# Optimization experiments

Measured on AMD Instinct MI355X. Metric: run time of the kernel, lower is better.

The kernel has to match this reference:

```python
import jax, jax.numpy as jnp
import numpy as np

LAYERS = 30
LPS = 10            # layers per stack (layers // stacks)
K = 3               # kernel size
RC = 64             # residual channels
GC = 128            # gate channels
SC = 64             # skip channels
AC = 80             # aux (mel) channels
DN = ('NCH', 'OIH', 'NCH')


def _conv1x1(w, x):
    # w: (O, I), x: (B, I, T) -> (B, O, T)
    return jnp.einsum('oi,bit->bot', w, x)


def setup_inputs() -> dict:
    key = jax.random.key(0)
    ks = jax.random.split(key, 10)
    B, T = 8, 8192
    s = 0.05
    f32 = jnp.float32
    inp = {
        'x': jax.random.normal(ks[0], (B, 1, T), f32),
        'x_mask': jnp.ones((B, 1, T), f32),
        'c': jax.random.normal(ks[1], (B, AC, T), f32),
        'first_w': jax.random.normal(ks[2], (RC, 1, 1), f32) * s,
        'first_b': jnp.zeros((RC,), f32),
        'conv_w': jax.random.normal(ks[3], (LAYERS, GC, RC, K), f32) * s,
        'conv_b': jnp.zeros((LAYERS, GC), f32),
        'aux_w': jax.random.normal(ks[4], (LAYERS, GC, AC), f32) * s,
        'out_w': jax.random.normal(ks[5], (LAYERS, RC + SC, GC // 2), f32) * s,
        'out_b': jnp.zeros((LAYERS, RC + SC), f32),
        'last_w1': jax.random.normal(ks[6], (SC, SC), f32) * s,
        'last_b1': jnp.zeros((SC,), f32),
        'last_w2': jax.random.normal(ks[7], (1, SC), f32) * s,
        'last_b2': jnp.zeros((1,), f32),
    }
    return inp


def reference(x, x_mask, c, first_w, first_b, conv_w, conv_b, aux_w,
              out_w, out_b, last_w1, last_b1, last_w2, last_b2):
    # first 1x1 conv: (B,1,T) -> (B,RC,T)
    x = jax.lax.conv_general_dilated(x, first_w, (1,), [(0, 0)],
                                     dimension_numbers=DN) + first_b[None, :, None]
    skips = jnp.zeros_like(x[:, :SC])  # (B, SC, T)
    for l in range(LAYERS):
        d = 2 ** (l % LPS)
        pad = (K - 1) // 2 * d
        residual = x
        # dilated conv (same padding): (B,RC,T) -> (B,GC,T)
        h = jax.lax.conv_general_dilated(x, conv_w[l], (1,), [(pad, pad)],
                                         rhs_dilation=(d,), dimension_numbers=DN)
        h = h + conv_b[l][None, :, None]
        # local conditioning 1x1 (no bias)
        h = h + _conv1x1(aux_w[l], c)
        xa, xb = jnp.split(h, 2, axis=1)          # (B, GC/2, T) each
        z = jnp.tanh(xa) * jax.nn.sigmoid(xb)     # gated activation
        o = _conv1x1(out_w[l], z) + out_b[l][None, :, None]  # (B, RC+SC, T)
        o = o * x_mask
        x = residual + o[:, :RC]
        skips = skips + o[:, RC:]
    # last_conv: ReLU -> 1x1 -> ReLU -> 1x1
    y = jax.nn.relu(skips)
    y = _conv1x1(last_w1, y) + last_b1[None, :, None]
    y = jax.nn.relu(y)
    y = _conv1x1(last_w2, y) + last_b2[None, :, None]
    return y
```

## Files before the change

### kernel.cpp

```cpp
#include <hip/hip_runtime.h>
#include <hip/hip_bf16.h>
#include <stdint.h>

#define T_LEN 8192
#define LAYERS 30

typedef __attribute__((ext_vector_type(8))) short bfx8;
typedef __attribute__((ext_vector_type(4))) float fx4;
typedef __attribute__((ext_vector_type(4))) int ix4;

static __device__ __forceinline__ unsigned short f2bf(float f) {
    union { float fv; unsigned u; } v; v.fv = f;
    unsigned r = v.u + 0x7fffu + ((v.u >> 16) & 1u);
    return (unsigned short)(r >> 16);
}
static __device__ __forceinline__ float bf2f(unsigned short u) {
    union { unsigned u; float f; } v; v.u = ((unsigned)u) << 16;
    return v.f;
}
static __device__ __forceinline__ unsigned pack2(float a, float b) {
    return (unsigned)f2bf(a) | ((unsigned)f2bf(b) << 16);
}

__global__ void pack_weights_k(const float* __restrict__ conv_w,
                               const float* __restrict__ aux_w,
                               const float* __restrict__ out_w,
                               unsigned short* __restrict__ wpack) {
    int tid = blockIdx.x * 256 + threadIdx.x;
    int lane = tid & 63;
    int f = (tid >> 6) % 88;
    int l = tid / (88 * 64);
    unsigned short vals[8];
#pragma unroll
    for (int j = 0; j < 8; j++) {
        int kl = ((lane >> 4) * 8) + j;
        float v;
        if (f < 72) {
            int ks = f >> 3, nf = f & 7;
            int g = nf * 16 + (lane & 15);
            if (ks < 6) {
                int tap = ks >> 1;
                int i = (ks & 1) * 32 + kl;
                v = conv_w[((l * 128 + g) * 64 + i) * 3 + tap];
            } else {
                int a = (ks - 6) * 32 + kl;
                v = (a < 80) ? aux_w[(l * 128 + g) * 80 + a] : 0.f;
            }
        } else {
            int fo = f - 72;
            int ks = fo >> 3, nf = fo & 7;
            int p = nf * 16 + (lane & 15);
            v = out_w[(l * 128 + p) * 64 + ks * 32 + kl];
        }
        vals[j] = f2bf(v);
    }
    unsigned* dst = (unsigned*)(wpack + (size_t)tid * 8);
    dst[0] = (unsigned)vals[0] | ((unsigned)vals[1] << 16);
    dst[1] = (unsigned)vals[2] | ((unsigned)vals[3] << 16);
    dst[2] = (unsigned)vals[4] | ((unsigned)vals[5] << 16);
    dst[3] = (unsigned)vals[6] | ((unsigned)vals[7] << 16);
}

__global__ void prep_c_k(const float* __restrict__ c, unsigned short* __restrict__ cbf) {
    __shared__ float tile[80][65];
    int bid = blockIdx.x;
    int b = bid >> 7;
    int t0 = (bid & 127) << 6;
    for (int idx = threadIdx.x; idx < 80 * 64; idx += 256) {
        int a = idx >> 6, tt = idx & 63;
        tile[a][tt] = c[((size_t)(b * 80 + a)) * T_LEN + t0 + tt];
    }
    __syncthreads();
    for (int idx = threadIdx.x; idx < 64 * 96; idx += 256) {
        int tt = idx / 96, a = idx % 96;
        float v = (a < 80) ? tile[a][tt] : 0.f;
        cbf[((size_t)(b * T_LEN + t0 + tt)) * 96 + a] = f2bf(v);
    }
}

__global__ __launch_bounds__(256, 4) void layer_k(
    const float* __restrict__ xsrc,
    float* __restrict__ xdst,
    unsigned short* __restrict__ skipbf,
    const unsigned short* __restrict__ cbf,
    const float* __restrict__ xmask,
    const float* __restrict__ fw, const float* __restrict__ fb,
    const unsigned short* __restrict__ wl,
    const float* __restrict__ conv_b_l,
    const float* __restrict__ out_b_l,
    int d, int first)
{
    __shared__ char smem[40960];
    unsigned short* xtap  = (unsigned short*)smem;
    float*          sg_l  = (float*)smem;
    unsigned short* z_l   = (unsigned short*)(smem + 17408);
    float*          o_l   = (float*)smem;
    unsigned short* ctile = (unsigned short*)(smem + 27648);

    const int tid = threadIdx.x;
    const int lane = tid & 63;
    const int wv = tid >> 6;
    int bid = (((int)blockIdx.x & 7) * 128) + ((int)blockIdx.x >> 3);
    const int b = bid >> 7;
    const int t0 = (bid & 127) << 6;
    const long rowbase = (long)b * T_LEN;
    const int klane = (lane >> 4) * 8;
    const int mrow = lane & 15;
    const int trow = (lane >> 4) * 4;
    const int tq_t = tid >> 2;
    const int tq_q = tid & 3;

    float xc[16];
    if (first) {
        float xs = xsrc[rowbase + t0 + tq_t];
#pragma unroll
        for (int k = 0; k < 16; k++)
            xc[k] = fmaf(fw[tq_q * 16 + k], xs, fb[tq_q * 16 + k]);
    } else {
        const float4* src = (const float4*)(xsrc + ((rowbase + t0 + tq_t) << 6) + tq_q * 16);
#pragma unroll
        for (int k = 0; k < 4; k++) {
            float4 v = src[k];
            xc[k * 4] = v.x; xc[k * 4 + 1] = v.y; xc[k * 4 + 2] = v.z; xc[k * 4 + 3] = v.w;
        }
    }
    {
        unsigned pk[8];
#pragma unroll
        for (int k = 0; k < 8; k++) pk[k] = pack2(xc[k * 2], xc[k * 2 + 1]);
        unsigned short* dst = xtap + (64 + tq_t) * 72 + tq_q * 16;
        *(ix4*)dst       = *(const ix4*)&pk[0];
        *(ix4*)(dst + 8) = *(const ix4*)&pk[4];
    }
#pragma unroll
    for (int u = 0; u < 2; u++) {
        int idx = tid + u * 256;
        int tp = idx >> 8;
        int rem = idx & 255;
        int row = rem >> 2, qq = rem & 3;
        int tg = t0 + row + (tp ? d : -d);
        float hv[16];
        if ((unsigned)tg < (unsigned)T_LEN) {
            if (first) {
                float xs = xsrc[rowbase + tg];
#pragma unroll
                for (int k = 0; k < 16; k++)
                    hv[k] = fmaf(fw[qq * 16 + k], xs, fb[qq * 16 + k]);
            } else {
                const float4* src = (const float4*)(xsrc + ((rowbase + tg) << 6) + qq * 16);
#pragma unroll
                for (int k = 0; k < 4; k++) {
                    float4 v = src[k];
                    hv[k * 4] = v.x; hv[k * 4 + 1] = v.y; hv[k * 4 + 2] = v.z; hv[k * 4 + 3] = v.w;
                }
            }
        } else {
#pragma unroll
            for (int k = 0; k < 16; k++) hv[k] = 0.f;
        }
        unsigned pk[8];
#pragma unroll
        for (int k = 0; k < 8; k++) pk[k] = pack2(hv[k * 2], hv[k * 2 + 1]);
        unsigned short* dst = xtap + (tp * 128 + row) * 72 + qq * 16;
        *(ix4*)dst       = *(const ix4*)&pk[0];
        *(ix4*)(dst + 8) = *(const ix4*)&pk[4];
    }
    for (int idx = tid; idx < 768; idx += 256) {
        int row = idx / 12, seg = idx % 12;
        ix4 v = *(const ix4*)(cbf + (rowbase + t0 + row) * 96 + seg * 8);
        *(ix4*)(ctile + row * 104 + seg * 8) = v;
    }

    bfx8 bq[2][2];
#pragma unroll
    for (int pk = 0; pk < 2; pk++)
#pragma unroll
        for (int n = 0; n < 2; n++)
            bq[pk][n] = *(const bfx8*)(wl + (size_t)((pk * 8 + wv * 2 + n) * 64 + lane) * 8);
    __syncthreads();

    fx4 acc[4][2];
#pragma unroll
    for (int m = 0; m < 4; m++) {
        acc[m][0] = (fx4){0.f, 0.f, 0.f, 0.f};
        acc[m][1] = (fx4){0.f, 0.f, 0.f, 0.f};
    }
#pragma unroll
    for (int ks = 0; ks < 9; ks++) {
        const unsigned short* abase; int off, stride;
        if (ks < 6) { abase = xtap + (ks >> 1) * (64 * 72); off = (ks & 1) * 32; stride = 72; }
        else        { abase = ctile;                        off = (ks - 6) * 32; stride = 104; }
        bfx8 af[4];
#pragma unroll
        for (int m = 0; m < 4; m++)
            af[m] = *(const bfx8*)(abase + (m * 16 + mrow) * stride + off + klane);
        bfx8 b0 = bq[ks & 1][0], b1 = bq[ks & 1][1];
        if (ks + 2 < 9) {
#pragma unroll
            for (int n = 0; n < 2; n++)
                bq[ks & 1][n] = *(const bfx8*)(wl + (size_t)(((ks + 2) * 8 + wv * 2 + n) * 64 + lane) * 8);
        }
#pragma unroll
        for (int m = 0; m < 4; m++) {
            acc[m][0] = __builtin_amdgcn_mfma_f32_16x16x32_bf16(af[m], b0, acc[m][0], 0, 0, 0);
            acc[m][1] = __builtin_amdgcn_mfma_f32_16x16x32_bf16(af[m], b1, acc[m][1], 0, 0, 0);
        }
    }
    __syncthreads();

    {
        float cb0 = conv_b_l[wv * 32 + mrow];
        float cb1 = conv_b_l[wv * 32 + 16 + mrow];
        if (wv >= 2) {
#pragma unroll
            for (int n = 0; n < 2; n++) {
                int col = (wv - 2) * 32 + n * 16 + mrow;
                float cb = n ? cb1 : cb0;
#pragma unroll
                for (int m = 0; m < 4; m++)
#pragma unroll
                    for (int r = 0; r < 4; r++) {
                        float h = acc[m][n][r] + cb;
                        sg_l[(m * 16 + trow + r) * 68 + col] = 1.f / (1.f + __expf(-h));
                    }
            }
        } else {
#pragma unroll
            for (int n = 0; n < 2; n++) {
                float cb = n ? cb1 : cb0;
#pragma unroll
                for (int m = 0; m < 4; m++)
#pragma unroll
                    for (int r = 0; r < 4; r++) {
                        float h = acc[m][n][r] + cb;
                        float e2 = __expf(2.f * h);
                        acc[m][n][r] = 1.f - 2.f / (e2 + 1.f);
                    }
            }
        }
    }
    __syncthreads();

    bfx8 ob[2][2];
#pragma unroll
    for (int ks = 0; ks < 2; ks++)
#pragma unroll
        for (int n = 0; n < 2; n++)
            ob[ks][n] = *(const bfx8*)(wl + (size_t)(((72 + ks * 8) + (wv * 2 + n)) * 64 + lane) * 8);

    if (wv < 2) {
#pragma unroll
        for (int n = 0; n < 2; n++) {
            int col = wv * 32 + n * 16 + mrow;
#pragma unroll
            for (int m = 0; m < 4; m++)
#pragma unroll
                for (int r = 0; r < 4; r++) {
                    int t = m * 16 + trow + r;
                    z_l[t * 72 + col] = f2bf(acc[m][n][r] * sg_l[t * 68 + col]);
                }
        }
    }
    __syncthreads();

    fx4 acc2[4][2];
#pragma unroll
    for (int m = 0; m < 4; m++) {
        acc2[m][0] = (fx4){0.f, 0.f, 0.f, 0.f};
        acc2[m][1] = (fx4){0.f, 0.f, 0.f, 0.f};
    }
#pragma unroll
    for (int ks = 0; ks < 2; ks++) {
        bfx8 af[4];
#pragma unroll
        for (int m = 0; m < 4; m++)
            af[m] = *(const bfx8*)(z_l + (m * 16 + mrow) * 72 + ks * 32 + klane);
#pragma unroll
        for (int m = 0; m < 4; m++) {
            acc2[m][0] = __builtin_amdgcn_mfma_f32_16x16x32_bf16(af[m], ob[ks][0], acc2[m][0], 0, 0, 0);
            acc2[m][1] = __builtin_amdgcn_mfma_f32_16x16x32_bf16(af[m], ob[ks][1], acc2[m][1], 0, 0, 0);
        }
    }
    __syncthreads();

#pragma unroll
    for (int n = 0; n < 2; n++) {
        int p = wv * 32 + n * 16 + mrow;
        float ob_ = out_b_l[p];
#pragma unroll
        for (int m = 0; m < 4; m++)
#pragma unroll
            for (int r = 0; r < 4; r++) {
                int t = m * 16 + trow + r;
                o_l[t * 132 + p] = acc2[m][n][r] + ob_;
            }
    }
    __syncthreads();

    {
        float mk = xmask[rowbase + t0 + tq_t];
        long ro = (rowbase + t0 + tq_t) << 6;
        const float* osrc = o_l + tq_t * 132;
        float* xp = xdst + ro + tq_q * 16;
#pragma unroll
        for (int k2 = 0; k2 < 4; k2++) {
            float4 o4 = *(const float4*)(osrc + tq_q * 16 + k2 * 4);
            float4 xv;
            xv.x = fmaf(o4.x, mk, xc[k2 * 4 + 0]);
            xv.y = fmaf(o4.y, mk, xc[k2 * 4 + 1]);
            xv.z = fmaf(o4.z, mk, xc[k2 * 4 + 2]);
            xv.w = fmaf(o4.w, mk, xc[k2 * 4 + 3]);
            *(float4*)(xp + k2 * 4) = xv;
        }
        unsigned short* sp = skipbf + ro + tq_q * 16;
        float sv[16];
        if (first) {
#pragma unroll
            for (int k = 0; k < 16; k++)
                sv[k] = osrc[64 + tq_q * 16 + k] * mk;
        } else {
            ix4 old0 = *(const ix4*)sp;
            ix4 old1 = *(const ix4*)(sp + 8);
            const unsigned short* op = (const unsigned short*)&old0;
            const unsigned short* op1 = (const unsigned short*)&old1;
#pragma unroll
            for (int k = 0; k < 8; k++)
                sv[k] = fmaf(osrc[64 + tq_q * 16 + k], mk, bf2f(op[k]));
#pragma unroll
            for (int k = 0; k < 8; k++)
                sv[8 + k] = fmaf(osrc[64 + tq_q * 16 + 8 + k], mk, bf2f(op1[k]));
        }
        unsigned pk[8];
#pragma unroll
        for (int k = 0; k < 8; k++) pk[k] = pack2(sv[k * 2], sv[k * 2 + 1]);
        *(ix4*)sp       = *(const ix4*)&pk[0];
        *(ix4*)(sp + 8) = *(const ix4*)&pk[4];
    }
}

__global__ __launch_bounds__(256) void final_k(
        const unsigned short* __restrict__ skipbf,
        const float* __restrict__ w1, const float* __restrict__ b1,
        const float* __restrict__ w2, const float* __restrict__ b2,
        float* __restrict__ out) {
    __shared__ float w1s[4096];
    __shared__ float b1s[64];
    __shared__ float w2s[64];
    for (int i = threadIdx.x; i < 4096; i += 256) w1s[i] = w1[i];
    if (threadIdx.x < 64) {
        b1s[threadIdx.x] = b1[threadIdx.x];
        w2s[threadIdx.x] = w2[threadIdx.x];
    }
    __syncthreads();

    int pos = blockIdx.x * 256 + threadIdx.x;
    const ix4* rowp = (const ix4*)(skipbf + (size_t)pos * 64);
    float4 s[16];
#pragma unroll
    for (int j = 0; j < 8; j++) {
        ix4 v = rowp[j];
        const unsigned short* pv = (const unsigned short*)&v;
        s[j * 2]     = make_float4(fmaxf(bf2f(pv[0]), 0.f), fmaxf(bf2f(pv[1]), 0.f),
                                   fmaxf(bf2f(pv[2]), 0.f), fmaxf(bf2f(pv[3]), 0.f));
        s[j * 2 + 1] = make_float4(fmaxf(bf2f(pv[4]), 0.f), fmaxf(bf2f(pv[5]), 0.f),
                                   fmaxf(bf2f(pv[6]), 0.f), fmaxf(bf2f(pv[7]), 0.f));
    }
    float total = b2[0];
    for (int o = 0; o < 64; o++) {
        const float4* wr = (const float4*)(w1s + o * 64);
        float d0 = 0.f, d1 = 0.f, d2 = 0.f, d3 = 0.f;
#pragma unroll
        for (int j = 0; j < 16; j++) {
            float4 w = wr[j];
            d0 = fmaf(w.x, s[j].x, d0);
            d1 = fmaf(w.y, s[j].y, d1);
            d2 = fmaf(w.z, s[j].z, d2);
            d3 = fmaf(w.w, s[j].w, d3);
        }
        float dot = (d0 + d1) + (d2 + d3) + b1s[o];
        total = fmaf(w2s[o], fmaxf(dot, 0.f), total);
    }
    out[pos] = total;
}

extern "C" void kernel_launch(void* const* d_in, const int* in_sizes, int n_in,
                              void* d_out, int out_size, void* d_ws, size_t ws_size,
                              hipStream_t stream) {
    const float* x       = (const float*)d_in[0];
    const float* xmask   = (const float*)d_in[1];
    const float* c       = (const float*)d_in[2];
    const float* first_w = (const float*)d_in[3];
    const float* first_b = (const float*)d_in[4];
    const float* conv_w  = (const float*)d_in[5];
    const float* conv_b  = (const float*)d_in[6];
    const float* aux_w   = (const float*)d_in[7];
    const float* out_w   = (const float*)d_in[8];
    const float* out_b   = (const float*)d_in[9];
    const float* lw1     = (const float*)d_in[10];
    const float* lb1     = (const float*)d_in[11];
    const float* lw2     = (const float*)d_in[12];
    const float* lb2     = (const float*)d_in[13];
    float* out = (float*)d_out;

    char* ws = (char*)d_ws;
    float*          xfA    = (float*)(ws + 0);
    float*          xfB    = (float*)(ws + 16777216);
    unsigned short* skipbf = (unsigned short*)(ws + 33554432);
    unsigned short* cbf    = (unsigned short*)(ws + 41943040);
    unsigned short* wpack  = (unsigned short*)(ws + 54525952);

    pack_weights_k<<<660, 256, 0, stream>>>(conv_w, aux_w, out_w, wpack);
    prep_c_k<<<1024, 256, 0, stream>>>(c, cbf);

    const float* src = x;
    for (int l = 0; l < LAYERS; l++) {
        int d = 1 << (l % 10);
        float* dst = (l & 1) ? xfB : xfA;
        layer_k<<<1024, 256, 0, stream>>>(src, dst, skipbf, cbf, xmask,
                                          first_w, first_b,
                                          wpack + (size_t)l * 45056,
                                          conv_b + l * 128, out_b + l * 128,
                                          d, (l == 0) ? 1 : 0);
        src = dst;
    }
    final_k<<<256, 256, 0, stream>>>(skipbf, lw1, lb1, lw2, lb2, out);
}
```

Before: 795.1 us.

## Fuse all layers into one persistent kernel with grid barriers

```diff
diff --git a/kernel.cpp b/kernel.cpp
--- a/kernel.cpp
+++ b/kernel.cpp
@@ -8,25 +8,35 @@
 typedef __attribute__((ext_vector_type(8))) short bfx8;
 typedef __attribute__((ext_vector_type(4))) float fx4;
 typedef __attribute__((ext_vector_type(4))) int ix4;
+typedef unsigned long long u64;
 
 static __device__ __forceinline__ unsigned short f2bf(float f) {
     union { float fv; unsigned u; } v; v.fv = f;
     unsigned r = v.u + 0x7fffu + ((v.u >> 16) & 1u);
     return (unsigned short)(r >> 16);
 }
-static __device__ __forceinline__ float bf2f(unsigned short u) {
-    union { unsigned u; float f; } v; v.u = ((unsigned)u) << 16;
-    return v.f;
-}
 static __device__ __forceinline__ unsigned pack2(float a, float b) {
     return (unsigned)f2bf(a) | ((unsigned)f2bf(b) << 16);
+}
+static __device__ __forceinline__ u64 pack4(float a, float b, float c, float d) {
+    return (u64)pack2(a, b) | ((u64)pack2(c, d) << 32);
+}
+static __device__ __forceinline__ u64 aload(const unsigned short* p) {
+    return __hip_atomic_load((const u64*)p, __ATOMIC_RELAXED, __HIP_MEMORY_SCOPE_AGENT);
+}
+static __device__ __forceinline__ void astore(unsigned short* p, u64 v) {
+    __hip_atomic_store((u64*)p, v, __ATOMIC_RELAXED, __HIP_MEMORY_SCOPE_AGENT);
 }
 
 __global__ void pack_weights_k(const float* __restrict__ conv_w,
                                const float* __restrict__ aux_w,
                                const float* __restrict__ out_w,
-                               unsigned short* __restrict__ wpack) {
+                               unsigned short* __restrict__ wpack,
+                               unsigned* __restrict__ bar) {
+    if (blockIdx.x == 0)
+        for (int i = threadIdx.x; i < 2048; i += 256) bar[i] = 0u;
     int tid = blockIdx.x * 256 + threadIdx.x;
+    if (tid >= 168960) return;
     int lane = tid & 63;
     int f = (tid >> 6) % 88;
     int l = tid / (88 * 64);
@@ -78,17 +88,32 @@
     }
 }
 
-__global__ __launch_bounds__(256, 4) void layer_k(
-    const float* __restrict__ xsrc,
-    float* __restrict__ xdst,
-    unsigned short* __restrict__ skipbf,
+static __device__ __forceinline__ void gbar(unsigned* bar, int bid, unsigned target) {
+    __syncthreads();
+    if (threadIdx.x == 0) {
+        unsigned v = __hip_atomic_fetch_add(&bar[(bid & 63) << 5], 1u,
+                                            __ATOMIC_RELAXED, __HIP_MEMORY_SCOPE_AGENT);
+        if ((v & 15u) == 15u)
+            __hip_atomic_fetch_add(&bar[2047], 1u,
+                                   __ATOMIC_RELAXED, __HIP_MEMORY_SCOPE_AGENT);
+        while (__hip_atomic_load(&bar[2047], __ATOMIC_RELAXED,
+                                 __HIP_MEMORY_SCOPE_AGENT) < target)
+            __builtin_amdgcn_s_sleep(4);
+    }
+    __syncthreads();
+    __builtin_amdgcn_sched_barrier(0);
+}
+
+__global__ __launch_bounds__(256, 4) void mega_k(
+    const float* __restrict__ xin, const float* __restrict__ xmask,
     const unsigned short* __restrict__ cbf,
-    const float* __restrict__ xmask,
     const float* __restrict__ fw, const float* __restrict__ fb,
-    const unsigned short* __restrict__ wl,
-    const float* __restrict__ conv_b_l,
-    const float* __restrict__ out_b_l,
-    int d, int first)
+    const float* __restrict__ conv_b, const float* __restrict__ out_b,
+    const float* __restrict__ lw1, const float* __restrict__ lb1,
+    const float* __restrict__ lw2, const float* __restrict__ lb2,
+    unsigned short* __restrict__ xbfA, unsigned short* __restrict__ xbfB,
+    const unsigned short* __restrict__ wpack,
+    unsigned* __restrict__ bar, float* __restrict__ out)
 {
     __shared__ char smem[40960];
     unsigned short* xtap  = (unsigned short*)smem;
@@ -100,7 +125,7 @@
     const int tid = threadIdx.x;
     const int lane = tid & 63;
     const int wv = tid >> 6;
-    int bid = (((int)blockIdx.x & 7) * 128) + ((int)blockIdx.x >> 3);
+    const int bid = (((int)blockIdx.x & 7) * 128) + ((int)blockIdx.x >> 3);
     const int b = bid >> 7;
     const int t0 = (bid & 127) << 6;
     const long rowbase = (long)b * T_LEN;
@@ -110,277 +135,259 @@
     const int tq_t = tid >> 2;
     const int tq_q = tid & 3;
 
-    float xc[16];
-    if (first) {
-        float xs = xsrc[rowbase + t0 + tq_t];
-#pragma unroll
-        for (int k = 0; k < 16; k++)
-            xc[k] = fmaf(fw[tq_q * 16 + k], xs, fb[tq_q * 16 + k]);
-    } else {
-        const float4* src = (const float4*)(xsrc + ((rowbase + t0 + tq_t) << 6) + tq_q * 16);
-#pragma unroll
-        for (int k = 0; k < 4; k++) {
-            float4 v = src[k];
-            xc[k * 4] = v.x; xc[k * 4 + 1] = v.y; xc[k * 4 + 2] = v.z; xc[k * 4 + 3] = v.w;
-        }
-    }
-    {
-        unsigned pk[8];
-#pragma unroll
-        for (int k = 0; k < 8; k++) pk[k] = pack2(xc[k * 2], xc[k * 2 + 1]);
-        unsigned short* dst = xtap + (64 + tq_t) * 72 + tq_q * 16;
-        *(ix4*)dst       = *(const ix4*)&pk[0];
-        *(ix4*)(dst + 8) = *(const ix4*)&pk[4];
-    }
-#pragma unroll
-    for (int u = 0; u < 2; u++) {
-        int idx = tid + u * 256;
-        int tp = idx >> 8;
-        int rem = idx & 255;
-        int row = rem >> 2, qq = rem & 3;
-        int tg = t0 + row + (tp ? d : -d);
-        float hv[16];
-        if ((unsigned)tg < (unsigned)T_LEN) {
-            if (first) {
-                float xs = xsrc[rowbase + tg];
-#pragma unroll
-                for (int k = 0; k < 16; k++)
-                    hv[k] = fmaf(fw[qq * 16 + k], xs, fb[qq * 16 + k]);
-            } else {
-                const float4* src = (const float4*)(xsrc + ((rowbase + tg) << 6) + qq * 16);
-#pragma unroll
-                for (int k = 0; k < 4; k++) {
-                    float4 v = src[k];
-                    hv[k * 4] = v.x; hv[k * 4 + 1] = v.y; hv[k * 4 + 2] = v.z; hv[k * 4 + 3] = v.w;
-                }
-            }
-        } else {
-#pragma unroll
-            for (int k = 0; k < 16; k++) hv[k] = 0.f;
-        }
-        unsigned pk[8];
-#pragma unroll
-        for (int k = 0; k < 8; k++) pk[k] = pack2(hv[k * 2], hv[k * 2 + 1]);
-        unsigned short* dst = xtap + (tp * 128 + row) * 72 + qq * 16;
-        *(ix4*)dst       = *(const ix4*)&pk[0];
-        *(ix4*)(dst + 8) = *(const ix4*)&pk[4];
-    }
     for (int idx = tid; idx < 768; idx += 256) {
         int row = idx / 12, seg = idx % 12;
         ix4 v = *(const ix4*)(cbf + (rowbase + t0 + row) * 96 + seg * 8);
         *(ix4*)(ctile + row * 104 + seg * 8) = v;
     }
-
-    bfx8 bq[2][2];
-#pragma unroll
-    for (int pk = 0; pk < 2; pk++)
-#pragma unroll
-        for (int n = 0; n < 2; n++)
-            bq[pk][n] = *(const bfx8*)(wl + (size_t)((pk * 8 + wv * 2 + n) * 64 + lane) * 8);
+    if (tid < 64)
+        *(float*)(ctile + tid * 104 + 96) = xmask[rowbase + t0 + tid];
+    float xc[16];
+    {
+        float xs = xin[rowbase + t0 + tq_t];
+#pragma unroll
+        for (int k = 0; k < 16; k++)
+            xc[k] = fmaf(fw[tq_q * 16 + k], xs, fb[tq_q * 16 + k]);
+    }
+    fx4 racc[4][2];
+#pragma unroll
+    for (int m = 0; m < 4; m++) {
+        racc[m][0] = (fx4){0.f, 0.f, 0.f, 0.f};
+        racc[m][1] = (fx4){0.f, 0.f, 0.f, 0.f};
+    }
+    {
+        unsigned short* dst = xbfA + ((rowbase + t0 + tq_t) << 6) + tq_q * 16;
+#pragma unroll
+        for (int k2 = 0; k2 < 4; k2++)
+            astore(dst + k2 * 4, pack4(xc[k2 * 4], xc[k2 * 4 + 1],
+                                       xc[k2 * 4 + 2], xc[k2 * 4 + 3]));
+    }
+    gbar(bar, bid, 64u);
+
+#pragma unroll 1
+    for (int l = 0; l < LAYERS; l++) {
+        const unsigned short* cur = (l & 1) ? xbfB : xbfA;
+        unsigned short*       nxt = (l & 1) ? xbfA : xbfB;
+        const int d = 1 << (l % 10);
+        const unsigned short* wl = wpack + (size_t)l * 45056;
+
+#pragma unroll
+        for (int u = 0; u < 2; u++) {
+            int idx = tid + u * 256;
+            int tp = idx >> 8;
+            int rem = idx & 255;
+            int row = rem >> 2, qq = rem & 3;
+            int tg = t0 + row + (tp ? d : -d);
+            u64 a0 = 0, a1 = 0, a2 = 0, a3 = 0;
+            if ((unsigned)tg < (unsigned)T_LEN) {
+                const unsigned short* sp = cur + ((rowbase + tg) << 6) + qq * 16;
+                a0 = aload(sp); a1 = aload(sp + 4); a2 = aload(sp + 8); a3 = aload(sp + 12);
+            }
+            u64* dl = (u64*)(xtap + (tp * 128 + row) * 72 + qq * 16);
+            dl[0] = a0; dl[1] = a1; dl[2] = a2; dl[3] = a3;
+        }
+        {
+            u64* dc = (u64*)(xtap + (64 + tq_t) * 72 + tq_q * 16);
+#pragma unroll
+            for (int k2 = 0; k2 < 4; k2++)
+                dc[k2] = pack4(xc[k2 * 4], xc[k2 * 4 + 1], xc[k2 * 4 + 2], xc[k2 * 4 + 3]);
+        }
+        bfx8 bq[2][2];
+#pragma unroll
+        for (int pk = 0; pk < 2; pk++)
+#pragma unroll
+            for (int n = 0; n < 2; n++)
+                bq[pk][n] = *(const bfx8*)(wl + (size_t)((pk * 8 + wv * 2 + n) * 64 + lane) * 8);
+        __syncthreads();
+
+        fx4 acc[4][2];
+#pragma unroll
+        for (int m = 0; m < 4; m++) {
+            acc[m][0] = (fx4){0.f, 0.f, 0.f, 0.f};
+            acc[m][1] = (fx4){0.f, 0.f, 0.f, 0.f};
+        }
+#pragma unroll
+        for (int ks = 0; ks < 9; ks++) {
+            const unsigned short* abase; int off, stride;
+            if (ks < 6) { abase = xtap + (ks >> 1) * (64 * 72); off = (ks & 1) * 32; stride = 72; }
+            else        { abase = ctile;                        off = (ks - 6) * 32; stride = 104; }
+            bfx8 af[4];
+#pragma unroll
+            for (int m = 0; m < 4; m++)
+                af[m] = *(const bfx8*)(abase + (m * 16 + mrow) * stride + off + klane);
+            bfx8 b0 = bq[ks & 1][0], b1 = bq[ks & 1][1];
+            if (ks + 2 < 9) {
+#pragma unroll
+                for (int n = 0; n < 2; n++)
+                    bq[ks & 1][n] = *(const bfx8*)(wl + (size_t)(((ks + 2) * 8 + wv * 2 + n) * 64 + lane) * 8);
+            }
+#pragma unroll
+            for (int m = 0; m < 4; m++) {
+                acc[m][0] = __builtin_amdgcn_mfma_f32_16x16x32_bf16(af[m], b0, acc[m][0], 0, 0, 0);
+                acc[m][1] = __builtin_amdgcn_mfma_f32_16x16x32_bf16(af[m], b1, acc[m][1], 0, 0, 0);
+            }
+        }
+        __syncthreads();
+
+        {
+            float cb0 = conv_b[l * 128 + wv * 32 + mrow];
+            float cb1 = conv_b[l * 128 + wv * 32 + 16 + mrow];
+            if (wv >= 2) {
+#pragma unroll
+                for (int n = 0; n < 2; n++) {
+                    int col = (wv - 2) * 32 + n * 16 + mrow;
+                    float cb = n ? cb1 : cb0;
+#pragma unroll
+                    for (int m = 0; m < 4; m++)
+#pragma unroll
+                        for (int r = 0; r < 4; r++) {
+                            float h = acc[m][n][r] + cb;
+                            sg_l[(m * 16 + trow + r) * 68 + col] = 1.f / (1.f + __expf(-h));
+                        }
+                }
+            } else {
+#pragma unroll
+                for (int n = 0; n < 2; n++) {
+                    float cb = n ? cb1 : cb0;
+#pragma unroll
+                    for (int m = 0; m < 4; m++)
+#pragma unroll
+                        for (int r = 0; r < 4; r++) {
+                            float h = acc[m][n][r] + cb;
+                            float e2 = __expf(2.f * h);
+                            acc[m][n][r] = 1.f - 2.f / (e2 + 1.f);
+                        }
+                }
+            }
+        }
+        __syncthreads();
+
+        bfx8 ob[2][2];
+#pragma unroll
+        for (int ks = 0; ks < 2; ks++)
+#pragma unroll
+            for (int n = 0; n < 2; n++)
+                ob[ks][n] = *(const bfx8*)(wl + (size_t)(((72 + ks * 8) + (wv * 2 + n)) * 64 + lane) * 8);
+
+        if (wv < 2) {
+#pragma unroll
+            for (int n = 0; n < 2; n++) {
+                int col = wv * 32 + n * 16 + mrow;
+#pragma unroll
+                for (int m = 0; m < 4; m++)
+#pragma unroll
+                    for (int r = 0; r < 4; r++) {
+                        int t = m * 16 + trow + r;
+                        z_l[t * 72 + col] = f2bf(acc[m][n][r] * sg_l[t * 68 + col]);
+                    }
+            }
+        }
+        __syncthreads();
+
+        fx4 acc2[4][2];
+#pragma unroll
+        for (int m = 0; m < 4; m++) {
+            acc2[m][0] = (fx4){0.f, 0.f, 0.f, 0.f};
+            acc2[m][1] = (fx4){0.f, 0.f, 0.f, 0.f};
+        }
+#pragma unroll
+        for (int ks = 0; ks < 2; ks++) {
+            bfx8 af[4];
+#pragma unroll
+            for (int m = 0; m < 4; m++)
+                af[m] = *(const bfx8*)(z_l + (m * 16 + mrow) * 72 + ks * 32 + klane);
+#pragma unroll
+            for (int m = 0; m < 4; m++) {
+                acc2[m][0] = __builtin_amdgcn_mfma_f32_16x16x32_bf16(af[m], ob[ks][0], acc2[m][0], 0, 0, 0);
+                acc2[m][1] = __builtin_amdgcn_mfma_f32_16x16x32_bf16(af[m], ob[ks][1], acc2[m][1], 0, 0, 0);
+            }
+        }
+        __syncthreads();
+
+        if (wv < 2) {
+#pragma unroll
+            for (int n = 0; n < 2; n++) {
+                int p = wv * 32 + n * 16 + mrow;
+                float ob_ = out_b[l * 128 + p];
+#pragma unroll
+                for (int m = 0; m < 4; m++)
+#pragma unroll
+                    for (int r = 0; r < 4; r++)
+                        o_l[(m * 16 + trow + r) * 68 + p] = acc2[m][n][r] + ob_;
+            }
+        } else {
+#pragma unroll
+            for (int n = 0; n < 2; n++) {
+                int p = wv * 32 + n * 16 + mrow;
+                float ob_ = out_b[l * 128 + p];
+#pragma unroll
+                for (int m = 0; m < 4; m++)
+#pragma unroll
+                    for (int r = 0; r < 4; r++) {
+                        int t = m * 16 + trow + r;
+                        float mk2 = *(const float*)(ctile + t * 104 + 96);
+                        racc[m][n][r] = fmaf(acc2[m][n][r] + ob_, mk2, racc[m][n][r]);
+                    }
+            }
+        }
+        __syncthreads();
+
+        {
+            float mkr = *(const float*)(ctile + tq_t * 104 + 96);
+            const float* osrc = o_l + tq_t * 68 + tq_q * 16;
+#pragma unroll
+            for (int k = 0; k < 16; k++)
+                xc[k] = fmaf(osrc[k], mkr, xc[k]);
+            if (l < LAYERS - 1) {
+                unsigned short* dst = nxt + ((rowbase + t0 + tq_t) << 6) + tq_q * 16;
+#pragma unroll
+                for (int k2 = 0; k2 < 4; k2++)
+                    astore(dst + k2 * 4, pack4(xc[k2 * 4], xc[k2 * 4 + 1],
+                                               xc[k2 * 4 + 2], xc[k2 * 4 + 3]));
+            }
+        }
+        if (l < LAYERS - 1)
+            gbar(bar, bid, 64u * (unsigned)(l + 2));
+    }
+
     __syncthreads();
-
-    fx4 acc[4][2];
-#pragma unroll
-    for (int m = 0; m < 4; m++) {
-        acc[m][0] = (fx4){0.f, 0.f, 0.f, 0.f};
-        acc[m][1] = (fx4){0.f, 0.f, 0.f, 0.f};
-    }
-#pragma unroll
-    for (int ks = 0; ks < 9; ks++) {
-        const unsigned short* abase; int off, stride;
-        if (ks < 6) { abase = xtap + (ks >> 1) * (64 * 72); off = (ks & 1) * 32; stride = 72; }
-        else        { abase = ctile;                        off = (ks - 6) * 32; stride = 104; }
-        bfx8 af[4];
-#pragma unroll
-        for (int m = 0; m < 4; m++)
-            af[m] = *(const bfx8*)(abase + (m * 16 + mrow) * stride + off + klane);
-        bfx8 b0 = bq[ks & 1][0], b1 = bq[ks & 1][1];
-        if (ks + 2 < 9) {
-#pragma unroll
-            for (int n = 0; n < 2; n++)
-                bq[ks & 1][n] = *(const bfx8*)(wl + (size_t)(((ks + 2) * 8 + wv * 2 + n) * 64 + lane) * 8);
-        }
-#pragma unroll
-        for (int m = 0; m < 4; m++) {
-            acc[m][0] = __builtin_amdgcn_mfma_f32_16x16x32_bf16(af[m], b0, acc[m][0], 0, 0, 0);
-            acc[m][1] = __builtin_amdgcn_mfma_f32_16x16x32_bf16(af[m], b1, acc[m][1], 0, 0, 0);
-        }
-    }
+    float* s_lds = (float*)smem;
+    float* w1s   = (float*)(smem + 17408);
+    float* b1s   = (float*)(smem + 33792);
+    float* w2s   = (float*)(smem + 34048);
+    if (wv >= 2) {
+#pragma unroll
+        for (int n = 0; n < 2; n++) {
+            int col = (wv - 2) * 32 + n * 16 + mrow;
+#pragma unroll
+            for (int m = 0; m < 4; m++)
+#pragma unroll
+                for (int r = 0; r < 4; r++)
+                    s_lds[(m * 16 + trow + r) * 68 + col] = racc[m][n][r];
+        }
+    }
+    for (int i = tid; i < 4096; i += 256)
+        w1s[(i & 63) * 64 + (i >> 6)] = lw1[i];
+    if (tid < 64) { b1s[tid] = lb1[tid]; w2s[tid] = lw2[tid]; }
     __syncthreads();
-
     {
-        float cb0 = conv_b_l[wv * 32 + mrow];
-        float cb1 = conv_b_l[wv * 32 + 16 + mrow];
-        if (wv >= 2) {
-#pragma unroll
-            for (int n = 0; n < 2; n++) {
-                int col = (wv - 2) * 32 + n * 16 + mrow;
-                float cb = n ? cb1 : cb0;
-#pragma unroll
-                for (int m = 0; m < 4; m++)
-#pragma unroll
-                    for (int r = 0; r < 4; r++) {
-                        float h = acc[m][n][r] + cb;
-                        sg_l[(m * 16 + trow + r) * 68 + col] = 1.f / (1.f + __expf(-h));
-                    }
-            }
-        } else {
-#pragma unroll
-            for (int n = 0; n < 2; n++) {
-                float cb = n ? cb1 : cb0;
-#pragma unroll
-                for (int m = 0; m < 4; m++)
-#pragma unroll
-                    for (int r = 0; r < 4; r++) {
-                        float h = acc[m][n][r] + cb;
-                        float e2 = __expf(2.f * h);
-                        acc[m][n][r] = 1.f - 2.f / (e2 + 1.f);
-                    }
-            }
-        }
-    }
-    __syncthreads();
-
-    bfx8 ob[2][2];
-#pragma unroll
-    for (int ks = 0; ks < 2; ks++)
-#pragma unroll
-        for (int n = 0; n < 2; n++)
-            ob[ks][n] = *(const bfx8*)(wl + (size_t)(((72 + ks * 8) + (wv * 2 + n)) * 64 + lane) * 8);
-
-    if (wv < 2) {
-#pragma unroll
-        for (int n = 0; n < 2; n++) {
-            int col = wv * 32 + n * 16 + mrow;
-#pragma unroll
-            for (int m = 0; m < 4; m++)
-#pragma unroll
-                for (int r = 0; r < 4; r++) {
-                    int t = m * 16 + trow + r;
-                    z_l[t * 72 + col] = f2bf(acc[m][n][r] * sg_l[t * 68 + col]);
-                }
-        }
-    }
-    __syncthreads();
-
-    fx4 acc2[4][2];
-#pragma unroll
-    for (int m = 0; m < 4; m++) {
-        acc2[m][0] = (fx4){0.f, 0.f, 0.f, 0.f};
-        acc2[m][1] = (fx4){0.f, 0.f, 0.f, 0.f};
-    }
-#pragma unroll
-    for (int ks = 0; ks < 2; ks++) {
-        bfx8 af[4];
-#pragma unroll
-        for (int m = 0; m < 4; m++)
-            af[m] = *(const bfx8*)(z_l + (m * 16 + mrow) * 72 + ks * 32 + klane);
-#pragma unroll
-        for (int m = 0; m < 4; m++) {
-            acc2[m][0] = __builtin_amdgcn_mfma_f32_16x16x32_bf16(af[m], ob[ks][0], acc2[m][0], 0, 0, 0);
-            acc2[m][1] = __builtin_amdgcn_mfma_f32_16x16x32_bf16(af[m], ob[ks][1], acc2[m][1], 0, 0, 0);
-        }
-    }
-    __syncthreads();
-
-#pragma unroll
-    for (int n = 0; n < 2; n++) {
-        int p = wv * 32 + n * 16 + mrow;
-        float ob_ = out_b_l[p];
-#pragma unroll
-        for (int m = 0; m < 4; m++)
-#pragma unroll
-            for (int r = 0; r < 4; r++) {
-                int t = m * 16 + trow + r;
-                o_l[t * 132 + p] = acc2[m][n][r] + ob_;
-            }
-    }
-    __syncthreads();
-
-    {
-        float mk = xmask[rowbase + t0 + tq_t];
-        long ro = (rowbase + t0 + tq_t) << 6;
-        const float* osrc = o_l + tq_t * 132;
-        float* xp = xdst + ro + tq_q * 16;
-#pragma unroll
-        for (int k2 = 0; k2 < 4; k2++) {
-            float4 o4 = *(const float4*)(osrc + tq_q * 16 + k2 * 4);
-            float4 xv;
-            xv.x = fmaf(o4.x, mk, xc[k2 * 4 + 0]);
-            xv.y = fmaf(o4.y, mk, xc[k2 * 4 + 1]);
-            xv.z = fmaf(o4.z, mk, xc[k2 * 4 + 2]);
-            xv.w = fmaf(o4.w, mk, xc[k2 * 4 + 3]);
-            *(float4*)(xp + k2 * 4) = xv;
-        }
-        unsigned short* sp = skipbf + ro + tq_q * 16;
-        float sv[16];
-        if (first) {
-#pragma unroll
-            for (int k = 0; k < 16; k++)
-                sv[k] = osrc[64 + tq_q * 16 + k] * mk;
-        } else {
-            ix4 old0 = *(const ix4*)sp;
-            ix4 old1 = *(const ix4*)(sp + 8);
-            const unsigned short* op = (const unsigned short*)&old0;
-            const unsigned short* op1 = (const unsigned short*)&old1;
-#pragma unroll
-            for (int k = 0; k < 8; k++)
-                sv[k] = fmaf(osrc[64 + tq_q * 16 + k], mk, bf2f(op[k]));
-#pragma unroll
-            for (int k = 0; k < 8; k++)
-                sv[8 + k] = fmaf(osrc[64 + tq_q * 16 + 8 + k], mk, bf2f(op1[k]));
-        }
-        unsigned pk[8];
-#pragma unroll
-        for (int k = 0; k < 8; k++) pk[k] = pack2(sv[k * 2], sv[k * 2 + 1]);
-        *(ix4*)sp       = *(const ix4*)&pk[0];
-        *(ix4*)(sp + 8) = *(const ix4*)&pk[4];
-    }
-}
-
-__global__ __launch_bounds__(256) void final_k(
-        const unsigned short* __restrict__ skipbf,
-        const float* __restrict__ w1, const float* __restrict__ b1,
-        const float* __restrict__ w2, const float* __restrict__ b2,
-        float* __restrict__ out) {
-    __shared__ float w1s[4096];
-    __shared__ float b1s[64];
-    __shared__ float w2s[64];
-    for (int i = threadIdx.x; i < 4096; i += 256) w1s[i] = w1[i];
-    if (threadIdx.x < 64) {
-        b1s[threadIdx.x] = b1[threadIdx.x];
-        w2s[threadIdx.x] = w2[threadIdx.x];
-    }
-    __syncthreads();
-
-    int pos = blockIdx.x * 256 + threadIdx.x;
-    const ix4* rowp = (const ix4*)(skipbf + (size_t)pos * 64);
-    float4 s[16];
-#pragma unroll
-    for (int j = 0; j < 8; j++) {
-        ix4 v = rowp[j];
-        const unsigned short* pv = (const unsigned short*)&v;
-        s[j * 2]     = make_float4(fmaxf(bf2f(pv[0]), 0.f), fmaxf(bf2f(pv[1]), 0.f),
-                                   fmaxf(bf2f(pv[2]), 0.f), fmaxf(bf2f(pv[3]), 0.f));
-        s[j * 2 + 1] = make_float4(fmaxf(bf2f(pv[4]), 0.f), fmaxf(bf2f(pv[5]), 0.f),
-                                   fmaxf(bf2f(pv[6]), 0.f), fmaxf(bf2f(pv[7]), 0.f));
-    }
-    float total = b2[0];
-    for (int o = 0; o < 64; o++) {
-        const float4* wr = (const float4*)(w1s + o * 64);
-        float d0 = 0.f, d1 = 0.f, d2 = 0.f, d3 = 0.f;
-#pragma unroll
-        for (int j = 0; j < 16; j++) {
-            float4 w = wr[j];
-            d0 = fmaf(w.x, s[j].x, d0);
-            d1 = fmaf(w.y, s[j].y, d1);
-            d2 = fmaf(w.z, s[j].z, d2);
-            d3 = fmaf(w.w, s[j].w, d3);
-        }
-        float dot = (d0 + d1) + (d2 + d3) + b1s[o];
-        total = fmaf(w2s[o], fmaxf(dot, 0.f), total);
-    }
-    out[pos] = total;
+        float accf[16];
+#pragma unroll
+        for (int oi = 0; oi < 16; oi++) accf[oi] = b1s[tq_q * 16 + oi];
+        for (int j = 0; j < 64; j++) {
+            float s = fmaxf(s_lds[tq_t * 68 + j], 0.f);
+            const float* wr = w1s + j * 64 + tq_q * 16;
+#pragma unroll
+            for (int oi = 0; oi < 16; oi++) accf[oi] = fmaf(wr[oi], s, accf[oi]);
+        }
+        float tot = 0.f;
+#pragma unroll
+        for (int oi = 0; oi < 16; oi++)
+            tot = fmaf(w2s[tq_q * 16 + oi], fmaxf(accf[oi], 0.f), tot);
+        tot += __shfl_xor(tot, 1);
+        tot += __shfl_xor(tot, 2);
+        if (tq_q == 0) out[rowbase + t0 + tq_t] = tot + lb2[0];
+    }
 }
 
 extern "C" void kernel_launch(void* const* d_in, const int* in_sizes, int n_in,
@@ -400,28 +407,18 @@
     const float* lb1     = (const float*)d_in[11];
     const float* lw2     = (const float*)d_in[12];
     const float* lb2     = (const float*)d_in[13];
-    float* out = (float*)d_out;
+    float* outp = (float*)d_out;
 
     char* ws = (char*)d_ws;
-    float*          xfA    = (float*)(ws + 0);
-    float*          xfB    = (float*)(ws + 16777216);
-    unsigned short* skipbf = (unsigned short*)(ws + 33554432);
-    unsigned short* cbf    = (unsigned short*)(ws + 41943040);
-    unsigned short* wpack  = (unsigned short*)(ws + 54525952);
-
-    pack_weights_k<<<660, 256, 0, stream>>>(conv_w, aux_w, out_w, wpack);
+    unsigned short* xbfA  = (unsigned short*)(ws + 0);
+    unsigned short* xbfB  = (unsigned short*)(ws + 8388608);
+    unsigned short* cbf   = (unsigned short*)(ws + 16777216);
+    unsigned short* wpack = (unsigned short*)(ws + 29360128);
+    unsigned*       bar   = (unsigned*)(ws + 32063488);
+
+    pack_weights_k<<<660, 256, 0, stream>>>(conv_w, aux_w, out_w, wpack, bar);
     prep_c_k<<<1024, 256, 0, stream>>>(c, cbf);
-
-    const float* src = x;
-    for (int l = 0; l < LAYERS; l++) {
-        int d = 1 << (l % 10);
-        float* dst = (l & 1) ? xfB : xfA;
-        layer_k<<<1024, 256, 0, stream>>>(src, dst, skipbf, cbf, xmask,
-                                          first_w, first_b,
-                                          wpack + (size_t)l * 45056,
-                                          conv_b + l * 128, out_b + l * 128,
-                                          d, (l == 0) ? 1 : 0);
-        src = dst;
-    }
-    final_k<<<256, 256, 0, stream>>>(skipbf, lw1, lb1, lw2, lb2, out);
-}
+    mega_k<<<1024, 256, 0, stream>>>(x, xmask, cbf, first_w, first_b,
+                                     conv_b, out_b, lw1, lb1, lw2, lb2,
+                                     xbfA, xbfB, wpack, bar, outp);
+}
```

Measured after the change: 1.223 ms. 53.8% more time.
